# Kernel optimization log

Hardware: AMD Instinct MI355X
Metric: run time of the kernel (lower is better)

## Reference

```python
import math
import jax, jax.numpy as jnp
import numpy as np

NUM_BINS = 128
NUM_FREQS = 64
HEAD_DIM = 2 * NUM_FREQS
NUM_QUERIES = 16384
EPS = 1e-8


def setup_inputs() -> dict:
    key = jax.random.key(0)
    k1, k2 = jax.random.split(key, 2)
    Q = jax.random.normal(k1, (NUM_QUERIES, HEAD_DIM), dtype=jnp.float32)
    rotated_probes = jax.random.normal(k2, (NUM_BINS, HEAD_DIM), dtype=jnp.float32)
    # probes are expected pre-normalized
    rotated_probes = rotated_probes / (jnp.linalg.norm(rotated_probes, axis=-1, keepdims=True) + EPS)
    init_value = math.log(math.e - 1.0)  # softplus(init)=1
    q_weights_raw = jnp.full((NUM_BINS, NUM_FREQS), init_value, dtype=jnp.float32)
    q_magnitude_weights = jnp.zeros((NUM_BINS, NUM_FREQS), dtype=jnp.float32)
    q_bias = jnp.zeros((NUM_BINS,), dtype=jnp.float32)
    return {
        "Q": Q,
        "rotated_probes": rotated_probes,
        "q_weights_raw": q_weights_raw,
        "q_magnitude_weights": q_magnitude_weights,
        "q_bias": q_bias,
    }


def reference(Q, rotated_probes, q_weights_raw, q_magnitude_weights, q_bias):
    F = NUM_FREQS
    # L2 normalize Q
    norm = jnp.linalg.norm(Q, axis=-1, keepdims=True)
    Qn = Q / (norm + EPS)
    Q_real, Q_imag = Qn[:, :F], Qn[:, F:]            # (Nq, F)
    P_real, P_imag = rotated_probes[:, :F], rotated_probes[:, F:]  # (B, F)
    # broadcast per-frequency complex error and distance: (Nq, B, F)
    err_r = P_real[None, :, :] - Q_real[:, None, :]
    err_i = P_imag[None, :, :] - Q_imag[:, None, :]
    distance = jnp.sqrt(err_r * err_r + err_i * err_i + EPS)
    # magnitude features on normalized Q: (Nq, F)
    Q_mag = jnp.sqrt(Q_real * Q_real + Q_imag * Q_imag + EPS)
    eff_w = -jax.nn.softplus(q_weights_raw)          # (B, F), negative weights
    distance_term = jnp.einsum('qbf,bf->qb', distance, eff_w)
    magnitude_term = Q_mag @ q_magnitude_weights.T   # (Nq, B)
    return distance_term + magnitude_term + q_bias[None, :]
```

## Files before the change

kernel.cpp:

```cpp
#include <hip/hip_runtime.h>

#define NBINS 128
#define NFREQ 64
#define HDIM 128
#define NQ 16384
#define EPSF 1e-8f

typedef _Float16 h2 __attribute__((ext_vector_type(2)));
#define B2(x) __builtin_bit_cast(h2, (x))
#define U32(x) __builtin_bit_cast(unsigned, (x))

__device__ __forceinline__ h2 cvt_pk(float a, float b) {
  return __builtin_bit_cast(h2, __builtin_amdgcn_cvt_pkrtz(a, b));
}

#define WS_NEEDED (64 * 1024)

__global__ __launch_bounds__(256) void pack8(
    const float* __restrict__ probes,
    const float* __restrict__ wraw,
    const float* __restrict__ mw,
    unsigned* __restrict__ ws) {
  const int id = blockIdx.x * 256 + threadIdx.x;
  if (id >= 1024) return;
  const int c = id >> 7, b = id & 127;
  const float* pb = probes + b * HDIM + c * 8;
  const float* wb = wraw + b * NFREQ + c * 8;
  const float* mb = mw + b * NFREQ + c * 8;
  float pr[8], pi[8], w[8], m[8];
  *reinterpret_cast<float4*>(&pr[0]) = *reinterpret_cast<const float4*>(pb);
  *reinterpret_cast<float4*>(&pr[4]) = *reinterpret_cast<const float4*>(pb + 4);
  *reinterpret_cast<float4*>(&pi[0]) = *reinterpret_cast<const float4*>(pb + NFREQ);
  *reinterpret_cast<float4*>(&pi[4]) = *reinterpret_cast<const float4*>(pb + NFREQ + 4);
  *reinterpret_cast<float4*>(&w[0])  = *reinterpret_cast<const float4*>(wb);
  *reinterpret_cast<float4*>(&w[4])  = *reinterpret_cast<const float4*>(wb + 4);
  *reinterpret_cast<float4*>(&m[0])  = *reinterpret_cast<const float4*>(mb);
  *reinterpret_cast<float4*>(&m[4])  = *reinterpret_cast<const float4*>(mb + 4);
  unsigned ep[8], wp[4], mp[4];
  #pragma unroll
  for (int j = 0; j < 8; ++j) {
    h2 v = {(_Float16)pr[j], (_Float16)pi[j]};
    ep[j] = U32(v);
  }
  #pragma unroll
  for (int k = 0; k < 4; ++k) {
    float w0 = w[2 * k], w1 = w[2 * k + 1];
    float n0 = -(fmaxf(w0, 0.0f) + log1pf(expf(-fabsf(w0))));
    float n1 = -(fmaxf(w1, 0.0f) + log1pf(expf(-fabsf(w1))));
    h2 vw = {(_Float16)n0, (_Float16)n1};
    h2 vm = {(_Float16)m[2 * k], (_Float16)m[2 * k + 1]};
    wp[k] = U32(vw);
    mp[k] = U32(vm);
  }
  unsigned* EP = ws + (size_t)(c * 128 + b) * 8;
  *reinterpret_cast<uint4*>(EP)     = make_uint4(ep[0], ep[1], ep[2], ep[3]);
  *reinterpret_cast<uint4*>(EP + 4) = make_uint4(ep[4], ep[5], ep[6], ep[7]);
  unsigned* WP = ws + 8192 + (size_t)(c * 128 + b) * 4;
  *reinterpret_cast<uint4*>(WP) = make_uint4(wp[0], wp[1], wp[2], wp[3]);
  unsigned* MP = ws + 12288 + (size_t)(c * 128 + b) * 4;
  *reinterpret_cast<uint4*>(MP) = make_uint4(mp[0], mp[1], mp[2], mp[3]);
}

__global__ __launch_bounds__(128, 8) void scorer12(
    const float* __restrict__ Q,
    const unsigned* __restrict__ ws,
    const float* __restrict__ bias,
    float* __restrict__ out) {
  __shared__ __align__(16) unsigned qep[4 * 64];
  __shared__ __align__(16) unsigned qqm[4 * 32];
  __shared__ float part[4][2][64];
  const int t = threadIdx.x;
  const int qblk = blockIdx.x * 4;

  {
    const int q = t >> 5;
    const int seg = t & 31;
    const float* qp = Q + (size_t)(qblk + q) * HDIM + seg * 2;
    const float2 r = *reinterpret_cast<const float2*>(qp);
    const float2 i = *reinterpret_cast<const float2*>(qp + NFREQ);
    float s = r.x * r.x + r.y * r.y + i.x * i.x + i.y * i.y;
    s += __shfl_xor(s, 1, 32);
    s += __shfl_xor(s, 2, 32);
    s += __shfl_xor(s, 4, 32);
    s += __shfl_xor(s, 8, 32);
    s += __shfl_xor(s, 16, 32);
    const float inv = 1.0f / (__builtin_amdgcn_sqrtf(s) + EPSF);
    const float qr0 = r.x * inv, qi0 = i.x * inv;
    const float qr1 = r.y * inv, qi1 = i.y * inv;
    h2 e0 = {(_Float16)(-qr0), (_Float16)(-qi0)};
    h2 e1 = {(_Float16)(-qr1), (_Float16)(-qi1)};
    *reinterpret_cast<uint2*>(&qep[q * 64 + seg * 2]) = make_uint2(U32(e0), U32(e1));
    const float qm0 = __builtin_amdgcn_sqrtf(fmaf(qr0, qr0, fmaf(qi0, qi0, EPSF)));
    const float qm1 = __builtin_amdgcn_sqrtf(fmaf(qr1, qr1, fmaf(qi1, qi1, EPSF)));
    h2 vm = {(_Float16)qm0, (_Float16)qm1};
    qqm[q * 32 + seg] = U32(vm);
  }
  __syncthreads();

  const int lane = t & 63;
  const int fh = __builtin_amdgcn_readfirstlane(t >> 6);

  float acc[4][2];
  #pragma unroll
  for (int q = 0; q < 4; ++q) acc[q][0] = acc[q][1] = 0.0f;

  #pragma unroll 1
  for (int ci = 0; ci < 4; ++ci) {
    const int c = fh * 4 + ci;
    const unsigned* EPb = ws + (size_t)(c * 128 + lane) * 8;
    const unsigned* WPb = ws + 8192 + (size_t)(c * 128 + lane) * 4;
    const unsigned* MPb = ws + 12288 + (size_t)(c * 128 + lane) * 4;
    const uint4 e0a = *reinterpret_cast<const uint4*>(EPb);
    const uint4 e0b = *reinterpret_cast<const uint4*>(EPb + 4);
    const uint4 e1a = *reinterpret_cast<const uint4*>(EPb + 512);
    const uint4 e1b = *reinterpret_cast<const uint4*>(EPb + 516);
    const uint4 w0v = *reinterpret_cast<const uint4*>(WPb);
    const uint4 w1v = *reinterpret_cast<const uint4*>(WPb + 256);
    const uint4 m0v = *reinterpret_cast<const uint4*>(MPb);
    const uint4 m1v = *reinterpret_cast<const uint4*>(MPb + 256);
    const unsigned ep[2][8] = {
        {e0a.x, e0a.y, e0a.z, e0a.w, e0b.x, e0b.y, e0b.z, e0b.w},
        {e1a.x, e1a.y, e1a.z, e1a.w, e1b.x, e1b.y, e1b.z, e1b.w}};
    const unsigned wp[2][4] = {{w0v.x, w0v.y, w0v.z, w0v.w},
                               {w1v.x, w1v.y, w1v.z, w1v.w}};
    const unsigned mp[2][4] = {{m0v.x, m0v.y, m0v.z, m0v.w},
                               {m1v.x, m1v.y, m1v.z, m1v.w}};
    #pragma unroll
    for (int q = 0; q < 4; ++q) {
      #pragma unroll
      for (int half = 0; half < 2; ++half) {
        const uint4 qa = *reinterpret_cast<const uint4*>(&qep[q * 64 + c * 8 + half * 4]);
        const uint2 qm2 = *reinterpret_cast<const uint2*>(&qqm[q * 32 + c * 4 + half * 2]);
        const unsigned qe[4] = {qa.x, qa.y, qa.z, qa.w};
        const unsigned qmw[2] = {qm2.x, qm2.y};
        #pragma unroll
        for (int bc = 0; bc < 2; ++bc) {
          float da = acc[q][bc];
          #pragma unroll
          for (int fp = 0; fp < 2; ++fp) {
            const int wi = half * 4 + 2 * fp;
            h2 e0 = B2(ep[bc][wi])     + B2(qe[2 * fp]);
            h2 e1 = B2(ep[bc][wi + 1]) + B2(qe[2 * fp + 1]);
            float d0 = __builtin_amdgcn_fdot2(e0, e0, EPSF, false);
            float d1 = __builtin_amdgcn_fdot2(e1, e1, EPSF, false);
            h2 dp = cvt_pk(__builtin_amdgcn_sqrtf(d0), __builtin_amdgcn_sqrtf(d1));
            da = __builtin_amdgcn_fdot2(dp, B2(wp[bc][half * 2 + fp]), da, false);
            da = __builtin_amdgcn_fdot2(B2(qmw[fp]), B2(mp[bc][half * 2 + fp]), da, false);
          }
          acc[q][bc] = da;
        }
      }
    }
  }

  if (fh == 1) {
    #pragma unroll
    for (int q = 0; q < 4; ++q) {
      part[q][0][lane] = acc[q][0];
      part[q][1][lane] = acc[q][1];
    }
  }
  __syncthreads();
  if (fh == 0) {
    const float bias0 = bias[lane];
    const float bias1 = bias[64 + lane];
    #pragma unroll
    for (int q = 0; q < 4; ++q) {
      const size_t row = (size_t)(qblk + q) * NBINS;
      out[row + lane]      = acc[q][0] + part[q][0][lane] + bias0;
      out[row + 64 + lane] = acc[q][1] + part[q][1][lane] + bias1;
    }
  }
}

extern "C" void kernel_launch(void* const* d_in, const int* in_sizes, int n_in,
                              void* d_out, int out_size, void* d_ws, size_t ws_size,
                              hipStream_t stream) {
  const float* Q      = (const float*)d_in[0];
  const float* probes = (const float*)d_in[1];
  const float* wraw   = (const float*)d_in[2];
  const float* mw     = (const float*)d_in[3];
  const float* bias   = (const float*)d_in[4];
  float* out = (float*)d_out;
  unsigned* ws = (unsigned*)d_ws;

  pack8<<<4, 256, 0, stream>>>(probes, wraw, mw, ws);
  scorer12<<<NQ / 4, 128, 0, stream>>>(Q, ws, bias, out);
}
```

Before: 37.29 us.

## Precompute normalized Q in prologue kernel and split frequencies across four waves

Q normalization and fp16 packing move out of the scorer into a prologue kernel that writes a per-query-group packed buffer to workspace, in the same launch as the probe packing. The scorer then reads the precomputed query data directly from global memory with no shared staging or barrier. It uses 256 threads with four waves each covering a quarter of the frequency chunks, reducing three partial sums through shared memory. This shortens the per-wave serial loop and removes the normalization prologue, at the cost of an extra global round trip of the packed Q data and more scalar loads.

```diff
diff --git a/kernel.cpp b/kernel.cpp
--- a/kernel.cpp
+++ b/kernel.cpp
@@ -14,99 +14,124 @@
   return __builtin_bit_cast(h2, __builtin_amdgcn_cvt_pkrtz(a, b));
 }
 
-#define WS_NEEDED (64 * 1024)
-
-__global__ __launch_bounds__(256) void pack8(
+#define QB_WOFF 16384
+#define WS_NEEDED (((size_t)QB_WOFF + (size_t)NQ * 24) * 4)
+
+#define QN_BLOCKS 256
+#define PACK_BLOCKS 4
+
+__global__ __launch_bounds__(256) void prologue13(
+    const float* __restrict__ Q,
     const float* __restrict__ probes,
     const float* __restrict__ wraw,
     const float* __restrict__ mw,
     unsigned* __restrict__ ws) {
-  const int id = blockIdx.x * 256 + threadIdx.x;
-  if (id >= 1024) return;
-  const int c = id >> 7, b = id & 127;
-  const float* pb = probes + b * HDIM + c * 8;
-  const float* wb = wraw + b * NFREQ + c * 8;
-  const float* mb = mw + b * NFREQ + c * 8;
-  float pr[8], pi[8], w[8], m[8];
-  *reinterpret_cast<float4*>(&pr[0]) = *reinterpret_cast<const float4*>(pb);
-  *reinterpret_cast<float4*>(&pr[4]) = *reinterpret_cast<const float4*>(pb + 4);
-  *reinterpret_cast<float4*>(&pi[0]) = *reinterpret_cast<const float4*>(pb + NFREQ);
-  *reinterpret_cast<float4*>(&pi[4]) = *reinterpret_cast<const float4*>(pb + NFREQ + 4);
-  *reinterpret_cast<float4*>(&w[0])  = *reinterpret_cast<const float4*>(wb);
-  *reinterpret_cast<float4*>(&w[4])  = *reinterpret_cast<const float4*>(wb + 4);
-  *reinterpret_cast<float4*>(&m[0])  = *reinterpret_cast<const float4*>(mb);
-  *reinterpret_cast<float4*>(&m[4])  = *reinterpret_cast<const float4*>(mb + 4);
-  unsigned ep[8], wp[4], mp[4];
-  #pragma unroll
-  for (int j = 0; j < 8; ++j) {
-    h2 v = {(_Float16)pr[j], (_Float16)pi[j]};
-    ep[j] = U32(v);
-  }
-  #pragma unroll
-  for (int k = 0; k < 4; ++k) {
-    float w0 = w[2 * k], w1 = w[2 * k + 1];
-    float n0 = -(fmaxf(w0, 0.0f) + log1pf(expf(-fabsf(w0))));
-    float n1 = -(fmaxf(w1, 0.0f) + log1pf(expf(-fabsf(w1))));
-    h2 vw = {(_Float16)n0, (_Float16)n1};
-    h2 vm = {(_Float16)m[2 * k], (_Float16)m[2 * k + 1]};
-    wp[k] = U32(vw);
-    mp[k] = U32(vm);
-  }
-  unsigned* EP = ws + (size_t)(c * 128 + b) * 8;
-  *reinterpret_cast<uint4*>(EP)     = make_uint4(ep[0], ep[1], ep[2], ep[3]);
-  *reinterpret_cast<uint4*>(EP + 4) = make_uint4(ep[4], ep[5], ep[6], ep[7]);
-  unsigned* WP = ws + 8192 + (size_t)(c * 128 + b) * 4;
-  *reinterpret_cast<uint4*>(WP) = make_uint4(wp[0], wp[1], wp[2], wp[3]);
-  unsigned* MP = ws + 12288 + (size_t)(c * 128 + b) * 4;
-  *reinterpret_cast<uint4*>(MP) = make_uint4(mp[0], mp[1], mp[2], mp[3]);
-}
-
-__global__ __launch_bounds__(128, 8) void scorer12(
-    const float* __restrict__ Q,
+  const int blk = blockIdx.x;
+  const int t = threadIdx.x;
+  if (blk < QN_BLOCKS) {
+    const int l = t & 3;
+    const int q = blk * 64 + (t >> 2);
+    const float* qp = Q + (size_t)q * HDIM;
+    float re[16], im[16];
+    #pragma unroll
+    for (int k = 0; k < 4; ++k) {
+      *reinterpret_cast<float4*>(&re[k * 4]) =
+          *reinterpret_cast<const float4*>(qp + 16 * l + k * 4);
+      *reinterpret_cast<float4*>(&im[k * 4]) =
+          *reinterpret_cast<const float4*>(qp + NFREQ + 16 * l + k * 4);
+    }
+    float s = 0.0f;
+    #pragma unroll
+    for (int k = 0; k < 16; ++k) {
+      s = fmaf(re[k], re[k], s);
+      s = fmaf(im[k], im[k], s);
+    }
+    s += __shfl_xor(s, 1, 4);
+    s += __shfl_xor(s, 2, 4);
+    const float inv = 1.0f / (__builtin_amdgcn_sqrtf(s) + EPSF);
+    unsigned eq[16], qmw[8];
+    float qm[16];
+    #pragma unroll
+    for (int k = 0; k < 16; ++k) {
+      const float qr = re[k] * inv;
+      const float qi = im[k] * inv;
+      h2 v = {(_Float16)(-qr), (_Float16)(-qi)};
+      eq[k] = U32(v);
+      qm[k] = __builtin_amdgcn_sqrtf(fmaf(qr, qr, fmaf(qi, qi, EPSF)));
+    }
+    #pragma unroll
+    for (int p = 0; p < 8; ++p) {
+      h2 v = {(_Float16)qm[2 * p], (_Float16)qm[2 * p + 1]};
+      qmw[p] = U32(v);
+    }
+    unsigned* seg = ws + QB_WOFF + ((size_t)(q >> 2) * 4 + l) * 96 + (q & 3) * 24;
+    *reinterpret_cast<uint4*>(seg + 0)  = make_uint4(eq[0], eq[1], eq[2], eq[3]);
+    *reinterpret_cast<uint4*>(seg + 4)  = make_uint4(eq[4], eq[5], eq[6], eq[7]);
+    *reinterpret_cast<uint4*>(seg + 8)  = make_uint4(eq[8], eq[9], eq[10], eq[11]);
+    *reinterpret_cast<uint4*>(seg + 12) = make_uint4(eq[12], eq[13], eq[14], eq[15]);
+    *reinterpret_cast<uint4*>(seg + 16) = make_uint4(qmw[0], qmw[1], qmw[2], qmw[3]);
+    *reinterpret_cast<uint4*>(seg + 20) = make_uint4(qmw[4], qmw[5], qmw[6], qmw[7]);
+  } else {
+    const int id = (blk - QN_BLOCKS) * 256 + t;
+    if (id >= 1024) return;
+    const int c = id >> 7, b = id & 127;
+    const float* pb = probes + b * HDIM + c * 8;
+    const float* wb = wraw + b * NFREQ + c * 8;
+    const float* mb = mw + b * NFREQ + c * 8;
+    float pr[8], pi[8], w[8], m[8];
+    *reinterpret_cast<float4*>(&pr[0]) = *reinterpret_cast<const float4*>(pb);
+    *reinterpret_cast<float4*>(&pr[4]) = *reinterpret_cast<const float4*>(pb + 4);
+    *reinterpret_cast<float4*>(&pi[0]) = *reinterpret_cast<const float4*>(pb + NFREQ);
+    *reinterpret_cast<float4*>(&pi[4]) = *reinterpret_cast<const float4*>(pb + NFREQ + 4);
+    *reinterpret_cast<float4*>(&w[0])  = *reinterpret_cast<const float4*>(wb);
+    *reinterpret_cast<float4*>(&w[4])  = *reinterpret_cast<const float4*>(wb + 4);
+    *reinterpret_cast<float4*>(&m[0])  = *reinterpret_cast<const float4*>(mb);
+    *reinterpret_cast<float4*>(&m[4])  = *reinterpret_cast<const float4*>(mb + 4);
+    unsigned ep[8], wp[4], mp[4];
+    #pragma unroll
+    for (int j = 0; j < 8; ++j) {
+      h2 v = {(_Float16)pr[j], (_Float16)pi[j]};
+      ep[j] = U32(v);
+    }
+    #pragma unroll
+    for (int k = 0; k < 4; ++k) {
+      float w0 = w[2 * k], w1 = w[2 * k + 1];
+      float n0 = -(fmaxf(w0, 0.0f) + log1pf(expf(-fabsf(w0))));
+      float n1 = -(fmaxf(w1, 0.0f) + log1pf(expf(-fabsf(w1))));
+      h2 vw = {(_Float16)n0, (_Float16)n1};
+      h2 vm = {(_Float16)m[2 * k], (_Float16)m[2 * k + 1]};
+      wp[k] = U32(vw);
+      mp[k] = U32(vm);
+    }
+    unsigned* EP = ws + (size_t)(c * 128 + b) * 8;
+    *reinterpret_cast<uint4*>(EP)     = make_uint4(ep[0], ep[1], ep[2], ep[3]);
+    *reinterpret_cast<uint4*>(EP + 4) = make_uint4(ep[4], ep[5], ep[6], ep[7]);
+    unsigned* WP = ws + 8192 + (size_t)(c * 128 + b) * 4;
+    *reinterpret_cast<uint4*>(WP) = make_uint4(wp[0], wp[1], wp[2], wp[3]);
+    unsigned* MP = ws + 12288 + (size_t)(c * 128 + b) * 4;
+    *reinterpret_cast<uint4*>(MP) = make_uint4(mp[0], mp[1], mp[2], mp[3]);
+  }
+}
+
+__global__ __launch_bounds__(256, 8) void scorer13(
     const unsigned* __restrict__ ws,
     const float* __restrict__ bias,
     float* __restrict__ out) {
-  __shared__ __align__(16) unsigned qep[4 * 64];
-  __shared__ __align__(16) unsigned qqm[4 * 32];
-  __shared__ float part[4][2][64];
+  __shared__ float part[3][4][2][64];
   const int t = threadIdx.x;
-  const int qblk = blockIdx.x * 4;
-
-  {
-    const int q = t >> 5;
-    const int seg = t & 31;
-    const float* qp = Q + (size_t)(qblk + q) * HDIM + seg * 2;
-    const float2 r = *reinterpret_cast<const float2*>(qp);
-    const float2 i = *reinterpret_cast<const float2*>(qp + NFREQ);
-    float s = r.x * r.x + r.y * r.y + i.x * i.x + i.y * i.y;
-    s += __shfl_xor(s, 1, 32);
-    s += __shfl_xor(s, 2, 32);
-    s += __shfl_xor(s, 4, 32);
-    s += __shfl_xor(s, 8, 32);
-    s += __shfl_xor(s, 16, 32);
-    const float inv = 1.0f / (__builtin_amdgcn_sqrtf(s) + EPSF);
-    const float qr0 = r.x * inv, qi0 = i.x * inv;
-    const float qr1 = r.y * inv, qi1 = i.y * inv;
-    h2 e0 = {(_Float16)(-qr0), (_Float16)(-qi0)};
-    h2 e1 = {(_Float16)(-qr1), (_Float16)(-qi1)};
-    *reinterpret_cast<uint2*>(&qep[q * 64 + seg * 2]) = make_uint2(U32(e0), U32(e1));
-    const float qm0 = __builtin_amdgcn_sqrtf(fmaf(qr0, qr0, fmaf(qi0, qi0, EPSF)));
-    const float qm1 = __builtin_amdgcn_sqrtf(fmaf(qr1, qr1, fmaf(qi1, qi1, EPSF)));
-    h2 vm = {(_Float16)qm0, (_Float16)qm1};
-    qqm[q * 32 + seg] = U32(vm);
-  }
-  __syncthreads();
-
   const int lane = t & 63;
-  const int fh = __builtin_amdgcn_readfirstlane(t >> 6);
+  const int fq = __builtin_amdgcn_readfirstlane(t >> 6);
+  const int g = blockIdx.x;
+
+  const unsigned* qd = ws + QB_WOFF + ((size_t)g * 4 + fq) * 96;
 
   float acc[4][2];
   #pragma unroll
   for (int q = 0; q < 4; ++q) acc[q][0] = acc[q][1] = 0.0f;
 
   #pragma unroll 1
-  for (int ci = 0; ci < 4; ++ci) {
-    const int c = fh * 4 + ci;
+  for (int ci = 0; ci < 2; ++ci) {
+    const int c = fq * 2 + ci;
     const unsigned* EPb = ws + (size_t)(c * 128 + lane) * 8;
     const unsigned* WPb = ws + 8192 + (size_t)(c * 128 + lane) * 4;
     const unsigned* MPb = ws + 12288 + (size_t)(c * 128 + lane) * 4;
@@ -129,23 +154,34 @@
     for (int q = 0; q < 4; ++q) {
       #pragma unroll
       for (int half = 0; half < 2; ++half) {
-        const uint4 qa = *reinterpret_cast<const uint4*>(&qep[q * 64 + c * 8 + half * 4]);
-        const uint2 qm2 = *reinterpret_cast<const uint2*>(&qqm[q * 32 + c * 4 + half * 2]);
-        const unsigned qe[4] = {qa.x, qa.y, qa.z, qa.w};
-        const unsigned qmw[2] = {qm2.x, qm2.y};
+        const unsigned qe0 = qd[q * 24 + ci * 8 + half * 4 + 0];
+        const unsigned qe1 = qd[q * 24 + ci * 8 + half * 4 + 1];
+        const unsigned qe2 = qd[q * 24 + ci * 8 + half * 4 + 2];
+        const unsigned qe3 = qd[q * 24 + ci * 8 + half * 4 + 3];
+        const unsigned qm0 = qd[q * 24 + 16 + ci * 4 + half * 2 + 0];
+        const unsigned qm1 = qd[q * 24 + 16 + ci * 4 + half * 2 + 1];
         #pragma unroll
         for (int bc = 0; bc < 2; ++bc) {
           float da = acc[q][bc];
-          #pragma unroll
-          for (int fp = 0; fp < 2; ++fp) {
-            const int wi = half * 4 + 2 * fp;
-            h2 e0 = B2(ep[bc][wi])     + B2(qe[2 * fp]);
-            h2 e1 = B2(ep[bc][wi + 1]) + B2(qe[2 * fp + 1]);
+          {
+            const int wi = half * 4;
+            h2 e0 = B2(ep[bc][wi])     + B2(qe0);
+            h2 e1 = B2(ep[bc][wi + 1]) + B2(qe1);
             float d0 = __builtin_amdgcn_fdot2(e0, e0, EPSF, false);
             float d1 = __builtin_amdgcn_fdot2(e1, e1, EPSF, false);
             h2 dp = cvt_pk(__builtin_amdgcn_sqrtf(d0), __builtin_amdgcn_sqrtf(d1));
-            da = __builtin_amdgcn_fdot2(dp, B2(wp[bc][half * 2 + fp]), da, false);
-            da = __builtin_amdgcn_fdot2(B2(qmw[fp]), B2(mp[bc][half * 2 + fp]), da, false);
+            da = __builtin_amdgcn_fdot2(dp, B2(wp[bc][half * 2]), da, false);
+            da = __builtin_amdgcn_fdot2(B2(qm0), B2(mp[bc][half * 2]), da, false);
+          }
+          {
+            const int wi = half * 4 + 2;
+            h2 e0 = B2(ep[bc][wi])     + B2(qe2);
+            h2 e1 = B2(ep[bc][wi + 1]) + B2(qe3);
+            float d0 = __builtin_amdgcn_fdot2(e0, e0, EPSF, false);
+            float d1 = __builtin_amdgcn_fdot2(e1, e1, EPSF, false);
+            h2 dp = cvt_pk(__builtin_amdgcn_sqrtf(d0), __builtin_amdgcn_sqrtf(d1));
+            da = __builtin_amdgcn_fdot2(dp, B2(wp[bc][half * 2 + 1]), da, false);
+            da = __builtin_amdgcn_fdot2(B2(qm1), B2(mp[bc][half * 2 + 1]), da, false);
           }
           acc[q][bc] = da;
         }
@@ -153,22 +189,26 @@
     }
   }
 
-  if (fh == 1) {
+  if (fq != 0) {
     #pragma unroll
     for (int q = 0; q < 4; ++q) {
-      part[q][0][lane] = acc[q][0];
-      part[q][1][lane] = acc[q][1];
+      part[fq - 1][q][0][lane] = acc[q][0];
+      part[fq - 1][q][1][lane] = acc[q][1];
     }
   }
   __syncthreads();
-  if (fh == 0) {
+  if (fq == 0) {
     const float bias0 = bias[lane];
     const float bias1 = bias[64 + lane];
     #pragma unroll
     for (int q = 0; q < 4; ++q) {
-      const size_t row = (size_t)(qblk + q) * NBINS;
-      out[row + lane]      = acc[q][0] + part[q][0][lane] + bias0;
-      out[row + 64 + lane] = acc[q][1] + part[q][1][lane] + bias1;
+      const size_t row = (size_t)(g * 4 + q) * NBINS;
+      float v0 = acc[q][0] + part[0][q][0][lane] + part[1][q][0][lane] +
+                 part[2][q][0][lane] + bias0;
+      float v1 = acc[q][1] + part[0][q][1][lane] + part[1][q][1][lane] +
+                 part[2][q][1][lane] + bias1;
+      out[row + lane] = v0;
+      out[row + 64 + lane] = v1;
     }
   }
 }
@@ -184,6 +224,6 @@
   float* out = (float*)d_out;
   unsigned* ws = (unsigned*)d_ws;
 
-  pack8<<<4, 256, 0, stream>>>(probes, wraw, mw, ws);
-  scorer12<<<NQ / 4, 128, 0, stream>>>(Q, ws, bias, out);
-}
+  prologue13<<<QN_BLOCKS + PACK_BLOCKS, 256, 0, stream>>>(Q, probes, wraw, mw, ws);
+  scorer13<<<NQ / 4, 256, 0, stream>>>(ws, bias, out);
+}
```

Measured after the change: 38.45 us. 3.1% more time.
